# Performance work log

Hardware: AMD Instinct MI355X
Metric: run time of the kernel (lower is better)

Reference implementation:

```python
import jax, jax.numpy as jnp
import numpy as np

N_NODES, N_EDGES = 5000, 50000
NUM_BASIS, CUTOFF, RADIAL_DIM = 8, 5.0, 64
NODE_EMBED, MAX_Z = 64, 100
NUM_NEIGHBORS = 10.0
PI = float(np.pi)

IRREPS_EDGE = [(1, 0, 1), (1, 1, -1), (1, 2, 1)]      # 1x0e + 1x1o + 1x2e (dim 9)
IRREPS_INIT = [(64, 0, 1)]                            # 64x0e
IRREPS_HID  = [(32, 0, 1), (16, 1, -1), (8, 2, 1)]    # 32x0e + 16x1o + 8x2e (dim 120)

def _offsets(irr):
    offs, o = [], 0
    for m, l, p in irr:
        offs.append(o); o += m * (2 * l + 1)
    return offs

def _sh_blocks(v, xp):
    # real spherical harmonics, component normalization, m = -l..l, v must be unit
    x, y, z = v[..., 0], v[..., 1], v[..., 2]
    s3, s5, s15 = 3.0 ** 0.5, 5.0 ** 0.5, 15.0 ** 0.5
    Y0 = xp.ones(v.shape[:-1] + (1,), dtype=v.dtype)
    Y1 = xp.stack([y, z, x], axis=-1) * s3
    Y2 = xp.stack([s15 * x * y, s15 * y * z, 0.5 * s5 * (3.0 * z * z - 1.0),
                   s15 * x * z, 0.5 * s15 * (x * x - y * y)], axis=-1)
    return [Y0, Y1, Y2]

def _rand_rot(rng):
    q, _ = np.linalg.qr(rng.normal(size=(3, 3)))
    if np.linalg.det(q) < 0:
        q[:, 0] = -q[:, 0]
    return q

def _wigner_D(l, R, pts):
    A = _sh_blocks(pts, np)[l]
    B = _sh_blocks(pts @ R.T, np)[l]
    return np.linalg.lstsq(A, B, rcond=None)[0].T  # Y(R r) = D @ Y(r)

def _cg(l1, l2, l3):
    # unit-norm real Clebsch-Gordan tensor from null space of rotation invariance
    rng = np.random.default_rng(1000 + 100 * l1 + 10 * l2 + l3)
    pts = rng.normal(size=(256, 3)); pts /= np.linalg.norm(pts, axis=1, keepdims=True)
    d1, d2, d3 = 2 * l1 + 1, 2 * l2 + 1, 2 * l3 + 1
    rows = []
    for _ in range(3):
        R = _rand_rot(rng)
        K = np.kron(np.kron(_wigner_D(l1, R, pts), _wigner_D(l2, R, pts)), _wigner_D(l3, R, pts))
        rows.append(K - np.eye(d1 * d2 * d3))
    _, _, Vt = np.linalg.svd(np.vstack(rows))
    C = Vt[-1].reshape(d1, d2, d3)
    i = np.argmax(np.abs(C))
    if C.flat[i] < 0:
        C = -C
    return (C / np.linalg.norm(C)).astype(np.float32)

def _make_paths(irreps_in, irreps_out):
    paths, off = [], 0
    fan = [0] * len(irreps_out)
    for i1, (m1, l1, p1) in enumerate(irreps_in):
        for i2, (m2, l2, p2) in enumerate(IRREPS_EDGE):
            for i3, (m3, l3, p3) in enumerate(irreps_out):
                if abs(l1 - l2) <= l3 <= l1 + l2 and p1 * p2 == p3:
                    paths.append((i1, i2, i3, off))
                    off += m1 * m2 * m3
                    fan[i3] += m1 * m2
    return paths, off, fan

PATHS0, NUMEL0, FAN0 = _make_paths(IRREPS_INIT, IRREPS_HID)   # NUMEL0 = 3584
PATHS1, NUMEL1, FAN1 = _make_paths(IRREPS_HID, IRREPS_HID)    # NUMEL1 = 3456

CG = {}
for _paths, _irr_in in ((PATHS0, IRREPS_INIT), (PATHS1, IRREPS_HID)):
    for _i1, _i2, _i3, _ in _paths:
        _key = (_irr_in[_i1][1], IRREPS_EDGE[_i2][1], IRREPS_HID[_i3][1])
        if _key not in CG:
            CG[_key] = jnp.asarray(_cg(*_key))

EDGE_OFF = _offsets(IRREPS_EDGE)

def _tensor_product(x, sh, w, irreps_in, irreps_out, paths, fan):
    E = x.shape[0]
    in_off = _offsets(irreps_in)
    outs = [jnp.zeros((E, m * (2 * l + 1)), x.dtype) for m, l, p in irreps_out]
    for i1, i2, i3, off in paths:
        m1, l1, _ = irreps_in[i1]
        _, l2, _ = IRREPS_EDGE[i2]
        m3, l3, _ = irreps_out[i3]
        x1 = x[:, in_off[i1]:in_off[i1] + m1 * (2 * l1 + 1)].reshape(E, m1, 2 * l1 + 1)
        y = sh[:, EDGE_OFF[i2]:EDGE_OFF[i2] + 2 * l2 + 1]
        wb = w[:, off:off + m1 * m3].reshape(E, m1, m3)
        alpha = (2 * l3 + 1) ** 0.5 / float(fan[i3]) ** 0.5
        msg = jnp.einsum('eui,ej,ijk,euv->evk', x1, y, CG[(l1, l2, l3)], wb) * alpha
        outs[i3] = outs[i3] + msg.reshape(E, -1)
    return jnp.concatenate(outs, axis=1)

def _self_connection(x, ws, irreps_in, irreps_out):
    N = x.shape[0]
    in_off = _offsets(irreps_in)
    outs, wi = [], 0
    for m3, l3, p3 in irreps_out:
        hit = [j for j, (m1, l1, p1) in enumerate(irreps_in) if (l1, p1) == (l3, p3)]
        if hit:
            j = hit[0]
            m1, l1, _ = irreps_in[j]
            xb = x[:, in_off[j]:in_off[j] + m1 * (2 * l1 + 1)].reshape(N, m1, 2 * l1 + 1)
            yb = jnp.einsum('nui,uv->nvi', xb, ws[wi]) / float(m1) ** 0.5
            outs.append(yb.reshape(N, -1)); wi += 1
        else:
            outs.append(jnp.zeros((N, m3 * (2 * l3 + 1)), x.dtype))
    return jnp.concatenate(outs, axis=1)

def _forward(positions, embed, rad_w1, rad_b1, rad_w2, rad_b2,
             wnn0_w1, wnn0_w2, wnn1_w1, wnn1_w2,
             sc0_0e, sc1_0e, sc1_1o, sc1_2e,
             edge_vec, edge_len, atomic_numbers, edge_index):
    node = embed[atomic_numbers]                                  # (N, 64)
    src, dst = edge_index[0], edge_index[1]
    u = edge_vec / (edge_len[:, None] + 1e-8)                     # unit edge vectors
    sh = jnp.concatenate(_sh_blocks(u, jnp), axis=-1)             # (E, 9)
    # radial basis encoding: Bessel basis * smooth cosine cutoff -> MLP
    freqs = jnp.arange(1, NUM_BASIS + 1, dtype=edge_len.dtype) * (PI / CUTOFF)
    r = edge_len[:, None]
    basis = jnp.sin(freqs * r) / jnp.maximum(r, 1e-8)
    xr = edge_len / CUTOFF
    cut = jnp.where(xr < 1.0, 0.5 * (1.0 + jnp.cos(PI * xr)), 0.0)
    rad = jax.nn.silu((basis * cut[:, None]) @ rad_w1 + rad_b1) @ rad_w2 + rad_b2
    inv_sqrt_n = 1.0 / NUM_NEIGHBORS ** 0.5
    layers = [(IRREPS_INIT, PATHS0, FAN0, wnn0_w1, wnn0_w2, [sc0_0e], True),
              (IRREPS_HID, PATHS1, FAN1, wnn1_w1, wnn1_w2, [sc1_0e, sc1_1o, sc1_2e], False)]
    for irr_in, paths, fan, w1, w2, scs, do_act in layers:
        w = jax.nn.silu(rad @ w1) @ w2                            # per-edge TP weights
        msg = _tensor_product(node[src], sh, w, irr_in, IRREPS_HID, paths, fan)
        agg = jax.ops.segment_sum(msg, dst, num_segments=N_NODES) * inv_sqrt_n
        node = agg + _self_connection(node, scs, irr_in, IRREPS_HID)
        if do_act:                                                # silu on L=0 scalars only
            node = jnp.concatenate([jax.nn.silu(node[:, :32]), node[:, 32:]], axis=1)
    return node                                                   # (N, 120)

def setup_inputs():
    key = jax.random.key(0)
    ks = jax.random.split(key, 20)
    edge_vec = jax.random.normal(ks[0], (N_EDGES, 3), jnp.float32) * 1.5
    edge_len = jnp.linalg.norm(edge_vec, axis=-1)
    return {
        'positions': jax.random.normal(ks[1], (N_NODES, 3), jnp.float32) * 5.0,
        'embed': jax.random.normal(ks[2], (MAX_Z, NODE_EMBED), jnp.float32),
        'rad_w1': jax.random.normal(ks[3], (NUM_BASIS, 64), jnp.float32) / NUM_BASIS ** 0.5,
        'rad_b1': jnp.zeros((64,), jnp.float32),
        'rad_w2': jax.random.normal(ks[4], (64, RADIAL_DIM), jnp.float32) / 8.0,
        'rad_b2': jnp.zeros((RADIAL_DIM,), jnp.float32),
        'wnn0_w1': jax.random.normal(ks[5], (RADIAL_DIM, 64), jnp.float32) / 8.0,
        'wnn0_w2': jax.random.normal(ks[6], (64, NUMEL0), jnp.float32) / 8.0,
        'wnn1_w1': jax.random.normal(ks[7], (RADIAL_DIM, 64), jnp.float32) / 8.0,
        'wnn1_w2': jax.random.normal(ks[8], (64, NUMEL1), jnp.float32) / 8.0,
        'sc0_0e': jax.random.normal(ks[9], (64, 32), jnp.float32),
        'sc1_0e': jax.random.normal(ks[10], (32, 32), jnp.float32),
        'sc1_1o': jax.random.normal(ks[11], (16, 16), jnp.float32),
        'sc1_2e': jax.random.normal(ks[12], (8, 8), jnp.float32),
        'edge_vec': edge_vec,
        'edge_len': edge_len,
        'atomic_numbers': jax.random.randint(ks[13], (N_NODES,), 0, MAX_Z, jnp.int32),
        'edge_index': jax.random.randint(ks[14], (2, N_EDGES), 0, N_NODES, jnp.int32),
    }

def reference(positions, embed, rad_w1, rad_b1, rad_w2, rad_b2,
              wnn0_w1, wnn0_w2, wnn1_w1, wnn1_w2,
              sc0_0e, sc1_0e, sc1_1o, sc1_2e,
              edge_vec, edge_len, atomic_numbers, edge_index):
    return _forward(positions, embed, rad_w1, rad_b1, rad_w2, rad_b2,
                    wnn0_w1, wnn0_w2, wnn1_w1, wnn1_w2,
                    sc0_0e, sc1_0e, sc1_1o, sc1_2e,
                    edge_vec, edge_len, atomic_numbers, edge_index)
```

## Files before the change

kernel.cpp:

```cpp
#include <hip/hip_runtime.h>
#include <hip/hip_bf16.h>
#include <math.h>

#define E_EDGES 50000
#define NN 5000

typedef __hip_bfloat16 bf16;
typedef __attribute__((ext_vector_type(8))) short short8;
typedef __attribute__((ext_vector_type(4))) float f32x4;

__device__ __forceinline__ float b2f(bf16 v) { return __bfloat162float(v); }
__device__ __forceinline__ float siluf(float x) { return x / (1.0f + __expf(-x)); }
__device__ __forceinline__ float us2f(unsigned short u) {
  union { unsigned int i; float f; } c; c.i = ((unsigned int)u) << 16; return c.f;
}

__global__ void __launch_bounds__(256) k_setup(
    const float* __restrict__ evec, const float* __restrict__ elen,
    float* __restrict__ shb, float* __restrict__ bc,
    const float* __restrict__ w2, const float* __restrict__ b2,
    const float* __restrict__ w01, const float* __restrict__ w11,
    bf16* __restrict__ Mbb,
    float* __restrict__ bias0, float* __restrict__ bias1,
    const float* __restrict__ emb, const int* __restrict__ an,
    float* __restrict__ node0, bf16* __restrict__ node0b,
    const float* __restrict__ w0, bf16* __restrict__ W0rtb,
    const float* __restrict__ w1w2, bf16* __restrict__ W2t,
    const int* __restrict__ ei, int* __restrict__ hist, int* __restrict__ hist2) {
  const int b = blockIdx.x, tid = threadIdx.x;
  if (b < 196) {
    int e = b*256 + tid;
    if (e >= E_EDGES) return;
    atomicAdd(&hist[ei[e]], 1);
    atomicAdd(&hist2[ei[E_EDGES + e]], 1);
    float x = evec[3*e+0], y = evec[3*e+1], z = evec[3*e+2];
    float r = elen[e];
    float inv = 1.0f / (r + 1e-8f);
    float ux = x*inv, uy = y*inv, uz = z*inv;
    const float s3 = 1.7320508075688772f, s5 = 2.2360679774997896f, s15 = 3.8729833462074170f;
    float* sh = shb + (size_t)e*12;
    sh[0] = 1.0f;
    sh[1] = s3*uy; sh[2] = s3*uz; sh[3] = s3*ux;
    sh[4] = s15*ux*uy; sh[5] = s15*uy*uz; sh[6] = 0.5f*s5*(3.0f*uz*uz - 1.0f);
    sh[7] = s15*ux*uz; sh[8] = 0.5f*s15*(ux*ux - uy*uy);
    sh[9] = 0.f; sh[10] = 0.f; sh[11] = 0.f;
    float rr = fmaxf(r, 1e-8f);
    const float pi = 3.14159265358979f;
    float xr = r * 0.2f;
    float cut = (xr < 1.0f) ? 0.5f*(1.0f + cosf(pi*xr)) : 0.0f;
    float fb = pi * 0.2f;
    for (int k = 1; k <= 8; ++k)
      bc[(size_t)e*8 + (k-1)] = sinf(fb*(float)k*r)/rr * cut;
  } else if (b < 212) {
    int i = (b-196)*256 + tid;
    int hh = i >> 6, c = i & 63;
    float a0 = 0.f, a1 = 0.f;
    for (int j = 0; j < 64; ++j) {
      float wv = w2[hh*64 + j];
      a0 += wv * w01[j*64 + c];
      a1 += wv * w11[j*64 + c];
    }
    Mbb[(size_t)c*64 + hh]        = __float2bfloat16(a0);
    Mbb[(size_t)(64 + c)*64 + hh] = __float2bfloat16(a1);
    if (hh == 0) {
      float s0 = 0.f, s1 = 0.f;
      for (int j = 0; j < 64; ++j) {
        s0 += b2[j] * w01[j*64 + c];
        s1 += b2[j] * w11[j*64 + c];
      }
      bias0[c] = s0;
      bias1[c] = s1;
    }
  } else if (b < 1462) {
    int i = (b-212)*256 + tid;
    int n = i >> 6, c = i & 63;
    float v = emb[an[n]*64 + c];
    node0[i] = v;
    node0b[i] = __float2bfloat16(v);
  } else if (b < 2358) {
    int idx = (b-1462)*256 + tid;
    int col = idx >> 6, u = idx & 63;
    int hh = col / 56, vp = col - hh*56;
    int boff, m3, v;
    if (vp < 32)      { boff = 0;    m3 = 32; v = vp; }
    else if (vp < 48) { boff = 2048; m3 = 16; v = vp - 32; }
    else              { boff = 3072; m3 = 8;  v = vp - 48; }
    W0rtb[idx] = __float2bfloat16(w0[hh*3584 + boff + u*m3 + v]);
  } else {
    int idx = (b-2358)*256 + tid;
    int nn = idx >> 6, k = idx & 63;
    int p, loc;
    if (nn < 1024)      { p=0;  loc=nn;      }
    else if (nn < 1536) { p=1;  loc=nn-1024; }
    else if (nn < 1792) { p=2;  loc=nn-1536; }
    else if (nn < 2048) { p=3;  loc=nn-1792; }
    else if (nn < 2560) { p=4;  loc=nn-2048; }
    else if (nn < 2688) { p=5;  loc=nn-2560; }
    else if (nn < 2944) { p=6;  loc=nn-2688; }
    else if (nn < 3008) { p=7;  loc=nn-2944; }
    else if (nn < 3136) { p=8;  loc=nn-3008; }
    else if (nn < 3392) { p=9;  loc=nn-3136; }
    else                { p=10; loc=nn-3392; }
    const int M1s[11] = {32,32,32,16,16,16,16,8,8,8,8};
    const int M3s[11] = {32,16,8,16,32,8,16,8,16,32,8};
    int m1 = M1s[p], m3 = M3s[p];
    int v = loc / m1, u = loc - v*m1;
    int src = (nn - loc) + u*m3 + v;
    W2t[idx] = __float2bfloat16(w1w2[(size_t)k*3456 + src]);
  }
}

__global__ void __launch_bounds__(256) k_mid(
    const float* __restrict__ bc,
    const float* __restrict__ w1, const float* __restrict__ b1,
    const bf16* __restrict__ Mbb,
    const float* __restrict__ bias0, const float* __restrict__ bias1,
    float* __restrict__ q0, bf16* __restrict__ q1b,
    const int* __restrict__ hist, int* __restrict__ start,
    const int* __restrict__ hist2, int* __restrict__ start2) {
  __shared__ float smem[1024];
  __shared__ __align__(16) short sHb[2048];
  const int tid = threadIdx.x;
  const int b = blockIdx.x;
  if (b < 1563) {
    float* sW1 = smem;
    float* sB  = smem + 512;
    float* sb0 = smem + 576;
    float* sb1 = smem + 640;
    float* sBC = smem + 704;
    const int j = tid >> 6, m = tid & 63;
    for (int i = tid; i < 512; i += 256) sW1[i] = w1[i];
    if (tid < 64) { sB[tid] = b1[tid]; sb0[tid] = bias0[tid]; sb1[tid] = bias1[tid]; }
    {
      int e = b*32 + (tid >> 3);
      int k = tid & 7;
      int eL = e < E_EDGES ? e : E_EDGES-1;
      sBC[tid] = bc[(size_t)eL*8 + k];
    }
    __syncthreads();
    #pragma unroll
    for (int g = 0; g < 8; ++g) {
      int el = g*4 + j;
      float t = sB[m];
      #pragma unroll
      for (int k = 0; k < 8; ++k) t += sBC[el*8+k]*sW1[k*64+m];
      bf16 hv = __float2bfloat16(siluf(t));
      sHb[el*64 + m] = *(short*)&hv;
    }
    __syncthreads();
    const int w = tid >> 6, lane = tid & 63;
    const int row16 = lane & 15, quad = lane >> 4;
    const int mtile = w & 1, cg = w >> 1;
    const short* ap = sHb + (mtile*16 + row16)*64 + quad*8;
    short8 a0 = *(const short8*)ap;
    short8 a1 = *(const short8*)(ap + 32);
    f32x4 acc[4] = {};
    #pragma unroll
    for (int ni = 0; ni < 4; ++ni) {
      const short* bp = (const short*)Mbb + (size_t)(cg*64 + ni*16 + row16)*64 + quad*8;
      short8 b0 = *(const short8*)bp;
      short8 b1v = *(const short8*)(bp + 32);
      acc[ni] = __builtin_amdgcn_mfma_f32_16x16x32_bf16(a0, b0, acc[ni], 0,0,0);
      acc[ni] = __builtin_amdgcn_mfma_f32_16x16x32_bf16(a1, b1v, acc[ni], 0,0,0);
    }
    const float* bias = cg ? sb1 : sb0;
    #pragma unroll
    for (int ni = 0; ni < 4; ++ni) {
      int c = ni*16 + row16;
      float bv = bias[c];
      #pragma unroll
      for (int r = 0; r < 4; ++r) {
        int e = b*32 + mtile*16 + quad*4 + r;
        if (e < E_EDGES) {
          float val = siluf(acc[ni][r] + bv);
          if (cg == 0) q0[(size_t)e*64 + c] = val;
          else         q1b[(size_t)e*64 + c] = __float2bfloat16(val);
        }
      }
    }
  } else {
    const int* h = (b == 1563) ? hist : hist2;
    int* st      = (b == 1563) ? start : start2;
    int* sp = (int*)smem;
    int base = tid*20;
    int localsum = 0;
    for (int i = 0; i < 20; ++i) { int jj = base+i; localsum += (jj < NN) ? h[jj] : 0; }
    sp[tid] = localsum;
    __syncthreads();
    if (tid == 0) {
      int acc = 0;
      for (int i = 0; i < 256; ++i) { int t = sp[i]; sp[i] = acc; acc += t; }
    }
    __syncthreads();
    int run = sp[tid];
    for (int i = 0; i < 20; ++i) {
      int jj = base+i;
      if (jj < NN) { st[jj] = run; run += h[jj]; }
    }
    if (tid == 255) st[NN] = run;
  }
}

__global__ void __launch_bounds__(256) k_pre0(
    const int* __restrict__ ei,
    const int* __restrict__ start, int* __restrict__ cursor, int* __restrict__ perm,
    const int* __restrict__ start2, int* __restrict__ cursor2, int* __restrict__ perm2,
    const bf16* __restrict__ A, const bf16* __restrict__ B, bf16* __restrict__ out) {
  __shared__ short lds[4][32*64];
  const int b = blockIdx.x, tid = threadIdx.x;
  if (b < 196) {
    int e = b*256 + tid;
    if (e >= E_EDGES) return;
    int src = ei[e];
    perm[start[src] + atomicAdd(&cursor[src], 1)] = e;
    int dst = ei[E_EDGES + e];
    perm2[start2[dst] + atomicAdd(&cursor2[dst], 1)] = e;
  } else {
    const int bb = b - 196;
    const int wid = tid >> 6, lane = tid & 63;
    const int nt = (bb % 14)*4 + wid;
    const int r0 = (bb / 14)*32;
    const int row16 = lane & 15, quad = lane >> 4;
    short8 a[2][2];
    #pragma unroll
    for (int mi = 0; mi < 2; ++mi) {
      int r = r0 + mi*16 + row16;
      int rg = (r < NN) ? r : 0;
      const short* ap = (const short*)A + (size_t)rg*64 + quad*8;
      a[mi][0] = *(const short8*)(ap);
      a[mi][1] = *(const short8*)(ap + 32);
    }
    if (nt < 56) {
      f32x4 acc[4][2] = {};
      #pragma unroll
      for (int ni = 0; ni < 4; ++ni) {
        int col = nt*64 + ni*16 + row16;
        const short* bp = (const short*)B + (size_t)col*64 + quad*8;
        short8 b0 = *(const short8*)(bp);
        short8 b1 = *(const short8*)(bp + 32);
        #pragma unroll
        for (int mi = 0; mi < 2; ++mi) {
          acc[ni][mi] = __builtin_amdgcn_mfma_f32_16x16x32_bf16(a[mi][0], b0, acc[ni][mi], 0,0,0);
          acc[ni][mi] = __builtin_amdgcn_mfma_f32_16x16x32_bf16(a[mi][1], b1, acc[ni][mi], 0,0,0);
        }
      }
      #pragma unroll
      for (int ni = 0; ni < 4; ++ni)
        #pragma unroll
        for (int mi = 0; mi < 2; ++mi)
          #pragma unroll
          for (int rr = 0; rr < 4; ++rr) {
            bf16 hv = __float2bfloat16(acc[ni][mi][rr]);
            lds[wid][(mi*16 + quad*4 + rr)*64 + ni*16 + row16] = *(short*)&hv;
          }
    }
    __syncthreads();
    if (nt < 56) {
      #pragma unroll
      for (int it = 0; it < 4; ++it) {
        int unit = it*64 + lane;
        int rrow = unit >> 3;
        int cu = (unit & 7) * 8;
        int r = r0 + rrow;
        if (r < NN)
          *(uint4*)((short*)out + (size_t)r*3584 + nt*64 + cu) =
              *(const uint4*)&lds[wid][rrow*64 + cu];
      }
    }
  }
}

__global__ void __launch_bounds__(256) k_msg0z(
    const float* __restrict__ q0, const bf16* __restrict__ G0,
    const int* __restrict__ start, const int* __restrict__ perm,
    float* __restrict__ zbuf) {
  __shared__ uint4 g4[448];
  __shared__ float sq[4][64];
  const int n = blockIdx.x;
  const int tid = threadIdx.x;
  const int wv = tid >> 6, lane = tid & 63;
  const uint4* gr = (const uint4*)(G0 + (size_t)n*3584);
  for (int i = tid; i < 448; i += 256) g4[i] = gr[i];
  const int s0 = start[n], s1 = start[n+1];
  __syncthreads();
  const short* gs = (const short*)g4;
  for (int base = s0; base < s1; base += 4) {
    int idx = base + wv;
    if (idx < s1) {
      int e = perm[idx];
      sq[wv][lane] = q0[(size_t)e*64 + lane];
      float z = 0.f;
      if (lane < 56) {
        #pragma unroll
        for (int h = 0; h < 64; ++h)
          z += sq[wv][h]*us2f((unsigned short)gs[h*56 + lane]);
        zbuf[(size_t)e*56 + lane] = z;
      }
    }
  }
}

__global__ void k_agg0(const float* __restrict__ zbuf, const float* __restrict__ shb,
                       const int* __restrict__ start2, const int* __restrict__ perm2,
                       const float* __restrict__ node0, const float* __restrict__ sc00,
                       float* __restrict__ node1) {
  __shared__ float n0[64];
  int n = blockIdx.x, tid = threadIdx.x;
  if (tid < 64) n0[tid] = node0[(size_t)n*64 + tid];
  __syncthreads();
  if (tid >= 120) return;
  int c = tid, zi, shi;
  if (c < 32)      { zi = c; shi = -1; }
  else if (c < 80) { int j = c-32, v = j/3, k = j - v*3; zi = 32 + v; shi = 1 + k; }
  else             { int j = c-80, v = j/5, k = j - v*5; zi = 48 + v; shi = 4 + k; }
  float acc = 0.f;
  const int s0 = start2[n], s1 = start2[n+1];
  for (int idx = s0; idx < s1; ++idx) {
    int e = perm2[idx];
    float z = zbuf[(size_t)e*56 + zi];
    acc += (shi < 0) ? z : z*shb[(size_t)e*12 + shi];
  }
  acc *= 0.125f * 0.3162277660168379f;
  if (c < 32) {
    float s = 0.f;
    for (int u = 0; u < 64; ++u) s += n0[u]*sc00[u*32 + c];
    acc += s * 0.125f;
    acc = siluf(acc);
  }
  node1[(size_t)n*120 + c] = acc;
}


static __device__ const int TM1[54] = {
  32,32,32,32,32,32,32,32,32,32,32,32,32,32,32,32,
  32,32,32,32,32,32,32,32,
  32,32,32,32,
  16,16,16,16,
  16,16,16,16,16,16,16,16,
  16,16,
  16,16,16,16,
  8,
  8,8,
  8,8,8,8,
  8};
static __device__ const int TNK[54] = {
  1,1,1,1,1,1,1,1,1,1,1,1,1,1,1,1,
  3,3,3,3,3,3,3,3,
  5,5,5,5,
  3,3,3,3,
  1,1,1,1,1,1,1,1,
  5,5,
  3,3,3,3,
  5,
  3,3,
  1,1,1,1,
  5};
static __device__ const int TTOF[54] = {
  0,0,0,0,0,0,0,0,0,0,0,0,0,0,0,0,
  32,32,32,32,32,32,32,32,
  128,128,128,128,
  288,288,288,288,
  336,336,336,336,336,336,336,336,
  352,352,
  432,432,432,432,
  480,
  520,520,
  544,544,544,544,
  552};
static __device__ const int TOUT[54] = {
  0,2,4,6,8,10,12,14,16,18,20,22,24,26,28,30,
  32,38,44,50,56,62,68,74,
  80,90,100,110,
  32,44,56,68,
  0,4,8,12,16,20,24,28,
  80,100,
  32,44,56,68,
  80,
  32,56,
  0,8,16,24,
  80};

#define US2F(s) us2f((unsigned short)(s))

#define DOT8(wa, wc, t8) \
  (wa[0]*US2F(t8[0]) + wa[1]*US2F(t8[1]) + wa[2]*US2F(t8[2]) + wa[3]*US2F(t8[3]) \
 + wc[0]*US2F(t8[4]) + wc[1]*US2F(t8[5]) + wc[2]*US2F(t8[6]) + wc[3]*US2F(t8[7]))

#define CH32(NKC, HALF) { \
    const int e = lane & 15, uq = lane >> 4; \
    const float* wb = wl + e*32; \
    const int sz = (e & 7) << 2; \
    const short* tb = tls16 + e*600 + toff + uq*8; \
    f32x4 wa = *(const f32x4*)&wb[(uq*8) ^ sz]; \
    f32x4 wc = *(const f32x4*)&wb[(uq*8 + 4) ^ sz]; \
    _Pragma("unroll") \
    for (int k = 0; k < NKC; ++k) { \
      short8 t8 = *(const short8*)(tb + k*32); \
      float ak = DOT8(wa, wc, t8); \
      ak += __shfl_xor(ak, 16); \
      ak += __shfl_xor(ak, 32); \
      if (uq == 0) atomicAdd(&msgl[e*121 + tout + (HALF)*(NKC) + k], ak); \
    } }

#define CH16(NKC, HALF) { \
    const int e = lane & 15, g = lane >> 4; \
    const int vll = g & 1, uh = (g >> 1) << 3; \
    const float* wb = wl + e*32; \
    const int sz = (e & 7) << 2; \
    const short* tb = tls16 + e*600 + toff + uh; \
    f32x4 wa = *(const f32x4*)&wb[(vll*16 + uh) ^ sz]; \
    f32x4 wc = *(const f32x4*)&wb[(vll*16 + uh + 4) ^ sz]; \
    _Pragma("unroll") \
    for (int k = 0; k < NKC; ++k) { \
      short8 t8 = *(const short8*)(tb + k*16); \
      float ak = DOT8(wa, wc, t8); \
      ak += __shfl_xor(ak, 32); \
      if (g < 2) atomicAdd(&msgl[e*121 + tout + ((HALF)*2 + vll)*(NKC) + k], ak); \
    } }

#define CH8(NKC, HALF) { \
    const int e = lane & 15, vll = lane >> 4; \
    const float* wb = wl + e*32; \
    const int sz = (e & 7) << 2; \
    const short* tb = tls16 + e*600 + toff; \
    f32x4 wa = *(const f32x4*)&wb[(vll*8) ^ sz]; \
    f32x4 wc = *(const f32x4*)&wb[(vll*8 + 4) ^ sz]; \
    _Pragma("unroll") \
    for (int k = 0; k < NKC; ++k) { \
      short8 t8 = *(const short8*)(tb + k*8); \
      float ak = DOT8(wa, wc, t8); \
      atomicAdd(&msgl[e*121 + tout + ((HALF)*4 + vll)*(NKC) + k], ak); \
    } }

#define STB(ST, VAL) { bf16 hv_ = __float2bfloat16(VAL); tp[ST] = *(short*)&hv_; }

__global__ void __launch_bounds__(256, 4) k_fuse(
    const bf16* __restrict__ q1b, const bf16* __restrict__ W2t,
    const float* __restrict__ node1, const float* __restrict__ shb,
    const int* __restrict__ ei, float* __restrict__ msg1) {
  __shared__ __align__(16) short tls16[16*600];
  __shared__ __align__(16) float wls[4*512];
  __shared__ float msgl[16*121];
  __shared__ float shl[16*12];
  float* xl = wls;

  const int tid = threadIdx.x;
  const int wv = tid >> 6, lane = tid & 63;
  const int e0 = blockIdx.x * 16;
  const int row16 = lane & 15, quad = lane >> 4;

  {
    int e = tid >> 4, c0 = tid & 15;
    int src = ei[e0 + e];
    const float* xp = node1 + (size_t)src*120;
    for (int c = c0; c < 120; c += 16) xl[e*120 + c] = xp[c];
    if (c0 < 12) shl[e*12 + c0] = shb[(size_t)(e0+e)*12 + c0];
  }
  for (int i = tid; i < 1936; i += 256) msgl[i] = 0.f;

  const short* ap = (const short*)q1b + (size_t)(e0 + row16)*64 + quad*8;
  short8 a0 = *(const short8*)ap;
  short8 a1 = *(const short8*)(ap + 32);

  __syncthreads();

  {
    const float Av = 0.3162277660168379f, Bc = 0.1825741858350554f, B2 = 0.3651483716701107f;
    const int I_[11] = {0,2,0,1,1,2, 0,1,2, 0,2};
    const int J_[11] = {2,0,1,0,2,1, 0,1,2, 0,2};
    const int K_[11] = {0,0,1,1,3,3, 2,2,2, 4,4};
    const float V_[11] = {Av,Av,Av,Av,Av,Av, -Bc,B2,-Bc, -Av,Av};
    const float P = 0.2390457218668787f, Q = 0.2070196678027063f, R = 0.1195228609334394f;
    const int I2_[25] = {0,0,2, 0,0,1,1,3,3, 1,1,2, 1,1,4, 2, 2,3,3, 2,4,4, 3,3,4};
    const int J2_[25] = {0,2,0, 1,3,0,3,0,1, 1,2,1, 1,4,1, 2, 3,2,3, 4,2,4, 3,4,3};
    const int K2_[25] = {2,0,0, 3,1,3,0,1,0, 2,1,1, 4,1,1, 2, 3,3,2, 4,4,2, 4,3,3};
    const float V2_[25] = {P,P,P, -Q,-Q,-Q,-Q,-Q,-Q, -R,-R,-R, Q,Q,Q, -P,
                           -R,-R,-R, P,P,P, -Q,-Q,-Q};

    if (wv == 0) {
      #pragma unroll
      for (int p = 0; p < 12; ++p) {
        int j = p*64 + lane;
        int e = j/48, r = j - e*48;
        int u = r/3, k = r - u*3;
        const float* x = xl + e*120;
        short* tp = tls16 + e*600;
        STB(288 + k*16 + u, x[32+u*3+k]*0.1178511301977579f);
      }
      #pragma unroll
      for (int p = 0; p < 4; ++p) {
        int j = p*64 + lane;
        int e = j >> 4, u = j & 15;
        const float* x = xl + e*120; const float* sh = shl + e*12;
        short* tp = tls16 + e*600;
        STB(336 + u, (x[32+u*3]*sh[1] + x[32+u*3+1]*sh[2] + x[32+u*3+2]*sh[3])
                     * 0.0771516749810460f);
      }
      #pragma unroll
      for (int p = 0; p < 2; ++p) {
        int j = p*64 + lane;
        int e = j >> 3, u = j & 7;
        const float* x = xl + e*120; const float* sh = shl + e*12;
        short* tp = tls16 + e*600;
        float y0 = x[80+u*5], y1 = x[80+u*5+1], y2 = x[80+u*5+2],
              y3 = x[80+u*5+3], y4 = x[80+u*5+4];
        float o0=0.f,o1=0.f,o2=0.f,o3=0.f,o4=0.f;
        #pragma unroll
        for (int q = 0; q < 25; ++q) {
          float xv = (I2_[q]==0) ? y0 : ((I2_[q]==1) ? y1 : ((I2_[q]==2) ? y2 :
                     ((I2_[q]==3) ? y3 : y4)));
          float term = V2_[q]*xv*sh[4+J2_[q]];
          if (K2_[q]==0) o0 += term; else if (K2_[q]==1) o1 += term;
          else if (K2_[q]==2) o2 += term; else if (K2_[q]==3) o3 += term; else o4 += term;
        }
        const float sc = 0.2795084971874737f;
        STB(552 + u, o0*sc); STB(552 + 8 + u, o1*sc); STB(552 + 16 + u, o2*sc);
        STB(552 + 24 + u, o3*sc); STB(552 + 32 + u, o4*sc);
      }
    } else if (wv == 1) {
      #pragma unroll
      for (int p = 0; p < 10; ++p) {
        int j = p*64 + lane;
        int e = j/40, r = j - e*40;
        int u = r/5, k = r - u*5;
        const float* x = xl + e*120;
        short* tp = tls16 + e*600;
        STB(480 + k*8 + u, x[80+u*5+k]*0.125f);
      }
      #pragma unroll
      for (int p = 0; p < 4; ++p) {
        int j = p*64 + lane;
        int e = j >> 4, u = j & 15;
        const float* x = xl + e*120; const float* sh = shl + e*12;
        short* tp = tls16 + e*600;
        float x0 = x[32+u*3], x1 = x[32+u*3+1], x2 = x[32+u*3+2];
        float o0=0.f,o1=0.f,o2=0.f,o3=0.f,o4=0.f;
        #pragma unroll
        for (int q = 0; q < 11; ++q) {
          float xv = (I_[q]==0) ? x0 : ((I_[q]==1) ? x1 : x2);
          float term = V_[q]*xv*sh[1+J_[q]];
          if (K_[q]==0) o0 += term; else if (K_[q]==1) o1 += term;
          else if (K_[q]==2) o2 += term; else if (K_[q]==3) o3 += term; else o4 += term;
        }
        const float sc = 0.2795084971874737f;
        STB(352 + u, o0*sc); STB(352 + 16 + u, o1*sc); STB(352 + 32 + u, o2*sc);
        STB(352 + 48 + u, o3*sc); STB(352 + 64 + u, o4*sc);
      }
      #pragma unroll
      for (int p = 0; p < 2; ++p) {
        int j = p*64 + lane;
        int e = j >> 3, u = j & 7;
        const float* x = xl + e*120; const float* sh = shl + e*12;
        short* tp = tls16 + e*600;
        STB(544 + u, (x[80+u*5]*sh[4] + x[80+u*5+1]*sh[5] + x[80+u*5+2]*sh[6]
                    + x[80+u*5+3]*sh[7] + x[80+u*5+4]*sh[8]) * 0.0597614304667197f);
      }
    } else if (wv == 2) {
      #pragma unroll
      for (int p = 0; p < 8; ++p) {
        int j = p*64 + lane;
        int e = j >> 5, u = j & 31;
        const float* x = xl + e*120;
        short* tp = tls16 + e*600;
        STB(u, x[u] * 0.1336306209562122f);
      }
      #pragma unroll
      for (int p = 0; p < 4; ++p) {
        int j = p*64 + lane;
        int e = j >> 4, u = j & 15;
        const float* x = xl + e*120; const float* sh = shl + e*12;
        short* tp = tls16 + e*600;
        float x0 = x[32+u*3], x1 = x[32+u*3+1], x2 = x[32+u*3+2];
        float o0=0.f,o1=0.f,o2=0.f;
        #pragma unroll
        for (int q = 0; q < 11; ++q) {
          float xv = (I_[q]==0) ? x0 : ((I_[q]==1) ? x1 : x2);
          float term = V_[q]*xv*sh[4+K_[q]];
          if (J_[q]==0) o0 += term; else if (J_[q]==1) o1 += term; else o2 += term;
        }
        const float sc = 0.2041241452319315f;
        STB(432 + u, o0*sc); STB(432 + 16 + u, o1*sc); STB(432 + 32 + u, o2*sc);
      }
      #pragma unroll
      for (int p = 0; p < 2; ++p) {
        int j = p*64 + lane;
        int e = j >> 3, u = j & 7;
        const float* x = xl + e*120; const float* sh = shl + e*12;
        short* tp = tls16 + e*600;
        float y0 = x[80+u*5], y1 = x[80+u*5+1], y2 = x[80+u*5+2],
              y3 = x[80+u*5+3], y4 = x[80+u*5+4];
        float o0=0.f,o1=0.f,o2=0.f;
        #pragma unroll
        for (int q = 0; q < 11; ++q) {
          float xv = (K_[q]==0) ? y0 : ((K_[q]==1) ? y1 : ((K_[q]==2) ? y2 :
                     ((K_[q]==3) ? y3 : y4)));
          float term = V_[q]*xv*sh[1+I_[q]];
          if (J_[q]==0) o0 += term; else if (J_[q]==1) o1 += term; else o2 += term;
        }
        const float sc = 0.2041241452319315f;
        STB(520 + u, o0*sc); STB(520 + 8 + u, o1*sc); STB(520 + 16 + u, o2*sc);
      }
    } else {
      #pragma unroll
      for (int p = 0; p < 8; ++p) {
        int j = p*64 + lane;
        int e = j >> 5, u = j & 31;
        const float* x = xl + e*120; const float* sh = shl + e*12;
        short* tp = tls16 + e*600;
        float xu = x[u];
        #pragma unroll
        for (int k = 0; k < 3; ++k)
          STB(32 + k*32 + u, xu*sh[1+k]*0.1178511301977579f);
      }
      #pragma unroll
      for (int p = 0; p < 8; ++p) {
        int j = p*64 + lane;
        int e = j >> 5, u = j & 31;
        const float* x = xl + e*120; const float* sh = shl + e*12;
        short* tp = tls16 + e*600;
        float xu = x[u];
        #pragma unroll
        for (int k = 0; k < 5; ++k)
          STB(128 + k*32 + u, xu*sh[4+k]*0.125f);
      }
    }
  }
  __syncthreads();

  float* wl = wls + wv*512;

  short8 bf0[4], bf1[4];
  {
    const int ntp = wv;
    #pragma unroll
    for (int ni = 0; ni < 4; ++ni) {
      const short* bp = (const short*)W2t + (size_t)(ntp*64 + ni*16 + row16)*64 + quad*8;
      bf0[ni] = *(const short8*)bp;
      bf1[ni] = *(const short8*)(bp + 32);
    }
  }

  for (int nt = wv; nt < 54; nt += 4) {
    f32x4 acc[4] = {};
    #pragma unroll
    for (int ni = 0; ni < 4; ++ni) {
      acc[ni] = __builtin_amdgcn_mfma_f32_16x16x32_bf16(a0, bf0[ni], acc[ni], 0,0,0);
      acc[ni] = __builtin_amdgcn_mfma_f32_16x16x32_bf16(a1, bf1[ni], acc[ni], 0,0,0);
    }
    if (nt + 4 < 54) {
      #pragma unroll
      for (int ni = 0; ni < 4; ++ni) {
        const short* bp = (const short*)W2t + (size_t)((nt+4)*64 + ni*16 + row16)*64 + quad*8;
        bf0[ni] = *(const short8*)bp;
        bf1[ni] = *(const short8*)(bp + 32);
      }
    }
    const int m1 = TM1[nt], nk = TNK[nt], toff = TTOF[nt], tout = TOUT[nt];
    #pragma unroll
    for (int half = 0; half < 2; ++half) {
      #pragma unroll
      for (int nh = 0; nh < 2; ++nh) {
        const int ni = half*2 + nh;
        #pragma unroll
        for (int r = 0; r < 4; ++r) {
          int e = quad*4 + r;
          int ch = nh*16 + row16;
          wl[e*32 + (ch ^ ((e & 7) << 2))] = acc[ni][r];
        }
      }
      if (m1 == 32) {
        if (nk == 1)      CH32(1, half)
        else if (nk == 3) CH32(3, half)
        else              CH32(5, half)
      } else if (m1 == 16) {
        if (nk == 1)      CH16(1, half)
        else if (nk == 3) CH16(3, half)
        else              CH16(5, half)
      } else {
        if (nk == 1)      CH8(1, half)
        else if (nk == 3) CH8(3, half)
        else              CH8(5, half)
      }
    }
  }

  __syncthreads();
  const float s = 0.3162277660168379f;
  for (int i = tid; i < 1920; i += 256) {
    int e = i / 120, c = i - e*120;
    msg1[(size_t)e0*120 + i] = msgl[e*121 + c] * s;
  }
}

__global__ void k_out(const float* __restrict__ msg1,
                      const int* __restrict__ start2, const int* __restrict__ perm2,
                      const float* __restrict__ node1,
                      const float* __restrict__ sc0e, const float* __restrict__ sc1o,
                      const float* __restrict__ sc2e, float* __restrict__ out) {
  __shared__ float x[120];
  int n = blockIdx.x, tid = threadIdx.x;
  if (tid < 120) x[tid] = node1[(size_t)n*120 + tid];
  __syncthreads();
  if (tid >= 120) return;
  float v = 0.f;
  const int s0 = start2[n], s1 = start2[n+1];
  for (int idx = s0; idx < s1; ++idx)
    v += msg1[(size_t)perm2[idx]*120 + tid];
  if (tid < 32) {
    float s = 0.f;
    for (int u = 0; u < 32; ++u) s += x[u]*sc0e[u*32 + tid];
    v += s * 0.1767766952966369f;
  } else if (tid < 80) {
    int jj = tid - 32, vv = jj/3, k = jj - vv*3;
    float s = 0.f;
    for (int u = 0; u < 16; ++u) s += x[32 + u*3 + k]*sc1o[u*16 + vv];
    v += s * 0.25f;
  } else {
    int jj = tid - 80, vv = jj/5, k = jj - vv*5;
    float s = 0.f;
    for (int u = 0; u < 8; ++u) s += x[80 + u*5 + k]*sc2e[u*8 + vv];
    v += s * 0.3535533905932738f;
  }
  out[(size_t)n*120 + tid] = v;
}

extern "C" void kernel_launch(void* const* d_in, const int* in_sizes, int n_in,
                              void* d_out, int out_size, void* d_ws, size_t ws_size,
                              hipStream_t stream) {
  const float* embed   = (const float*)d_in[1];
  const float* rad_w1  = (const float*)d_in[2];
  const float* rad_b1  = (const float*)d_in[3];
  const float* rad_w2  = (const float*)d_in[4];
  const float* rad_b2  = (const float*)d_in[5];
  const float* wnn0_w1 = (const float*)d_in[6];
  const float* wnn0_w2 = (const float*)d_in[7];
  const float* wnn1_w1 = (const float*)d_in[8];
  const float* wnn1_w2 = (const float*)d_in[9];
  const float* sc0_0e  = (const float*)d_in[10];
  const float* sc1_0e  = (const float*)d_in[11];
  const float* sc1_1o  = (const float*)d_in[12];
  const float* sc1_2e  = (const float*)d_in[13];
  const float* edge_vec = (const float*)d_in[14];
  const float* edge_len = (const float*)d_in[15];
  const int*  anum    = (const int*)d_in[16];
  const int*  ei      = (const int*)d_in[17];

  float* ws = (float*)d_ws;
  float* shbuf = ws;
  float* bc    = ws + 600000;
  bf16*  q1b   = (bf16*)(ws + 1000000);
  float* node0 = ws + 2600000;
  bf16*  node0b= (bf16*)(ws + 2920000);
  bf16*  W0rtb = (bf16*)(ws + 3080000);
  bf16*  W2t   = (bf16*)(ws + 3194688);
  bf16*  Mbb   = (bf16*)(ws + 3305280);
  float* bias0 = ws + 3309376;
  float* bias1 = ws + 3309440;
  int*   hist   = (int*)(ws + 3309504);
  int*   cursor = (int*)(ws + 3314504);
  int*   hist2  = (int*)(ws + 3319504);
  int*   cursor2= (int*)(ws + 3324504);
  int*   start  = (int*)(ws + 3329504);
  int*   start2 = (int*)(ws + 3334512);
  int*   perm   = (int*)(ws + 3339520);
  int*   perm2  = (int*)(ws + 3389520);
  float* node1 = ws + 3439520;
  float* msg1  = ws + 4039520;
  float* q0    = ws + 10039520;
  float* zbuf  = ws + 13239520;
  bf16*  G0    = (bf16*)(ws + 16039520);

  hipMemsetAsync(hist, 0, 20000*sizeof(int), stream);

  k_setup<<<3222, 256, 0, stream>>>(edge_vec, edge_len, shbuf, bc,
                                    rad_w2, rad_b2, wnn0_w1, wnn1_w1, Mbb, bias0, bias1,
                                    embed, anum, node0, node0b,
                                    wnn0_w2, W0rtb, wnn1_w2, W2t, ei, hist, hist2);
  k_mid<<<1565, 256, 0, stream>>>(bc, rad_w1, rad_b1, Mbb, bias0, bias1,
                                  q0, q1b, hist, start, hist2, start2);
  k_pre0<<<196 + 14*157, 256, 0, stream>>>(ei, start, cursor, perm,
                                           start2, cursor2, perm2,
                                           node0b, W0rtb, G0);
  k_msg0z<<<NN, 256, 0, stream>>>(q0, G0, start, perm, zbuf);
  k_agg0<<<NN, 128, 0, stream>>>(zbuf, shbuf, start2, perm2, node0, sc0_0e, node1);

  k_fuse<<<3125, 256, 0, stream>>>(q1b, W2t, node1, shbuf, ei, msg1);

  k_out<<<NN, 128, 0, stream>>>(msg1, start2, perm2, node1, sc1_0e, sc1_1o, sc1_2e, (float*)d_out);
}
```

Baseline: 408.5 us.

## Use fp16 dot2 contractions and software-pipeline MFMA tiles in k_fuse

Result: slower. 577.6 us (+41.4%).

```diff
diff --git a/kernel.cpp b/kernel.cpp
--- a/kernel.cpp
+++ b/kernel.cpp
@@ -8,11 +8,27 @@
 typedef __hip_bfloat16 bf16;
 typedef __attribute__((ext_vector_type(8))) short short8;
 typedef __attribute__((ext_vector_type(4))) float f32x4;
+typedef __attribute__((ext_vector_type(2))) _Float16 h2;
 
 __device__ __forceinline__ float b2f(bf16 v) { return __bfloat162float(v); }
 __device__ __forceinline__ float siluf(float x) { return x / (1.0f + __expf(-x)); }
 __device__ __forceinline__ float us2f(unsigned short u) {
   union { unsigned int i; float f; } c; c.i = ((unsigned int)u) << 16; return c.f;
+}
+
+__device__ __forceinline__ float fdot2f(h2 a, h2 b, float c) {
+#if __has_builtin(__builtin_amdgcn_fdot2)
+  return __builtin_amdgcn_fdot2(a, b, c, false);
+#else
+  return c + (float)a.x*(float)b.x + (float)a.y*(float)b.y;
+#endif
+}
+__device__ __forceinline__ float dot8h(uint4 w, uint4 t, float acc) {
+  acc = fdot2f(__builtin_bit_cast(h2, w.x), __builtin_bit_cast(h2, t.x), acc);
+  acc = fdot2f(__builtin_bit_cast(h2, w.y), __builtin_bit_cast(h2, t.y), acc);
+  acc = fdot2f(__builtin_bit_cast(h2, w.z), __builtin_bit_cast(h2, t.z), acc);
+  acc = fdot2f(__builtin_bit_cast(h2, w.w), __builtin_bit_cast(h2, t.w), acc);
+  return acc;
 }
 
 __global__ void __launch_bounds__(256) k_setup(
@@ -380,69 +396,81 @@
   0,8,16,24,
   80};
 
-#define US2F(s) us2f((unsigned short)(s))
-
-#define DOT8(wa, wc, t8) \
-  (wa[0]*US2F(t8[0]) + wa[1]*US2F(t8[1]) + wa[2]*US2F(t8[2]) + wa[3]*US2F(t8[3]) \
- + wc[0]*US2F(t8[4]) + wc[1]*US2F(t8[5]) + wc[2]*US2F(t8[6]) + wc[3]*US2F(t8[7]))
-
-#define CH32(NKC, HALF) { \
-    const int e = lane & 15, uq = lane >> 4; \
-    const float* wb = wl + e*32; \
-    const int sz = (e & 7) << 2; \
-    const short* tb = tls16 + e*600 + toff + uq*8; \
-    f32x4 wa = *(const f32x4*)&wb[(uq*8) ^ sz]; \
-    f32x4 wc = *(const f32x4*)&wb[(uq*8 + 4) ^ sz]; \
+#define STB(ST, VAL) { _Float16 hv_ = (_Float16)(VAL); tp[ST] = *(short*)&hv_; }
+
+#define STORE_WL(ACC) { \
     _Pragma("unroll") \
-    for (int k = 0; k < NKC; ++k) { \
-      short8 t8 = *(const short8*)(tb + k*32); \
-      float ak = DOT8(wa, wc, t8); \
-      ak += __shfl_xor(ak, 16); \
+    for (int ni_ = 0; ni_ < 4; ++ni_) { \
+      _Pragma("unroll") \
+      for (int r_ = 0; r_ < 4; ++r_) { \
+        int e_ = quad*4 + r_; \
+        int c_ = ni_*16 + row16; \
+        _Float16 hv_ = (_Float16)((ACC)[ni_][r_]); \
+        wl16[e_*64 + ((((c_>>3) ^ (e_&7))<<3) | (c_&7))] = *(short*)&hv_; \
+      } \
+    } }
+
+#define MFMA_STORE(NTT) { \
+    f32x4 acc_[4] = {}; \
+    _Pragma("unroll") \
+    for (int ni_ = 0; ni_ < 4; ++ni_) { \
+      acc_[ni_] = __builtin_amdgcn_mfma_f32_16x16x32_bf16(a0, bf0[ni_], acc_[ni_], 0,0,0); \
+      acc_[ni_] = __builtin_amdgcn_mfma_f32_16x16x32_bf16(a1, bf1[ni_], acc_[ni_], 0,0,0); \
+    } \
+    if ((NTT) + 4 < 54) { \
+      _Pragma("unroll") \
+      for (int ni_ = 0; ni_ < 4; ++ni_) { \
+        const short* bp_ = (const short*)W2t + (size_t)(((NTT)+4)*64 + ni_*16 + row16)*64 + quad*8; \
+        bf0[ni_] = *(const short8*)bp_; \
+        bf1[ni_] = *(const short8*)(bp_ + 32); \
+      } \
+    } \
+    STORE_WL(acc_) }
+
+#define LD2(NKC, STRIDE) \
+    _Pragma("unroll") \
+    for (int k_ = 0; k_ < NKC; ++k_) { \
+      tr[k_][0] = *(const uint4*)&tb[k_*(STRIDE)]; \
+      tr[k_][1] = *(const uint4*)&tb[k_*(STRIDE) + 8]; \
+    }
+#define LD1(NKC) \
+    _Pragma("unroll") \
+    for (int k_ = 0; k_ < NKC; ++k_) \
+      tr[k_][0] = *(const uint4*)&tb[k_*8];
+
+#define CP32(NKC) \
+    _Pragma("unroll") \
+    for (int k_ = 0; k_ < NKC; ++k_) { \
+      float ak = dot8h(wr0, tr[k_][0], 0.f); \
+      ak = dot8h(wr1, tr[k_][1], ak); \
       ak += __shfl_xor(ak, 32); \
-      if (uq == 0) atomicAdd(&msgl[e*121 + tout + (HALF)*(NKC) + k], ak); \
-    } }
-
-#define CH16(NKC, HALF) { \
-    const int e = lane & 15, g = lane >> 4; \
-    const int vll = g & 1, uh = (g >> 1) << 3; \
-    const float* wb = wl + e*32; \
-    const int sz = (e & 7) << 2; \
-    const short* tb = tls16 + e*600 + toff + uh; \
-    f32x4 wa = *(const f32x4*)&wb[(vll*16 + uh) ^ sz]; \
-    f32x4 wc = *(const f32x4*)&wb[(vll*16 + uh + 4) ^ sz]; \
+      if (g < 2) atomicAdd(&msgl[e*121 + tout + (g&1)*(NKC) + k_], ak); \
+    }
+#define CP16(NKC) \
     _Pragma("unroll") \
-    for (int k = 0; k < NKC; ++k) { \
-      short8 t8 = *(const short8*)(tb + k*16); \
-      float ak = DOT8(wa, wc, t8); \
-      ak += __shfl_xor(ak, 32); \
-      if (g < 2) atomicAdd(&msgl[e*121 + tout + ((HALF)*2 + vll)*(NKC) + k], ak); \
-    } }
-
-#define CH8(NKC, HALF) { \
-    const int e = lane & 15, vll = lane >> 4; \
-    const float* wb = wl + e*32; \
-    const int sz = (e & 7) << 2; \
-    const short* tb = tls16 + e*600 + toff; \
-    f32x4 wa = *(const f32x4*)&wb[(vll*8) ^ sz]; \
-    f32x4 wc = *(const f32x4*)&wb[(vll*8 + 4) ^ sz]; \
+    for (int k_ = 0; k_ < NKC; ++k_) { \
+      float ak = dot8h(wr0, tr[k_][0], 0.f); \
+      ak = dot8h(wr1, tr[k_][1], ak); \
+      atomicAdd(&msgl[e*121 + tout + g*(NKC) + k_], ak); \
+    }
+#define CP8(NKC) \
     _Pragma("unroll") \
-    for (int k = 0; k < NKC; ++k) { \
-      short8 t8 = *(const short8*)(tb + k*8); \
-      float ak = DOT8(wa, wc, t8); \
-      atomicAdd(&msgl[e*121 + tout + ((HALF)*4 + vll)*(NKC) + k], ak); \
-    } }
-
-#define STB(ST, VAL) { bf16 hv_ = __float2bfloat16(VAL); tp[ST] = *(short*)&hv_; }
+    for (int k_ = 0; k_ < NKC; ++k_) { \
+      float ak = dot8h(wr0, tr[k_][0], 0.f); \
+      atomicAdd(&msgl[e*121 + tout + g*(NKC) + k_], ak); \
+      float ak2 = dot8h(wr1, tr[k_][0], 0.f); \
+      atomicAdd(&msgl[e*121 + tout + (g+4)*(NKC) + k_], ak2); \
+    }
 
 __global__ void __launch_bounds__(256, 4) k_fuse(
     const bf16* __restrict__ q1b, const bf16* __restrict__ W2t,
     const float* __restrict__ node1, const float* __restrict__ shb,
     const int* __restrict__ ei, float* __restrict__ msg1) {
   __shared__ __align__(16) short tls16[16*600];
-  __shared__ __align__(16) float wls[4*512];
+  __shared__ __align__(16) short wls16[4*1024];
   __shared__ float msgl[16*121];
   __shared__ float shl[16*12];
-  float* xl = wls;
+  float* xl = (float*)wls16;
 
   const int tid = threadIdx.x;
   const int wv = tid >> 6, lane = tid & 63;
@@ -461,6 +489,13 @@
   const short* ap = (const short*)q1b + (size_t)(e0 + row16)*64 + quad*8;
   short8 a0 = *(const short8*)ap;
   short8 a1 = *(const short8*)(ap + 32);
+  short8 bf0[4], bf1[4];
+  #pragma unroll
+  for (int ni = 0; ni < 4; ++ni) {
+    const short* bp = (const short*)W2t + (size_t)(wv*64 + ni*16 + row16)*64 + quad*8;
+    bf0[ni] = *(const short8*)bp;
+    bf1[ni] = *(const short8*)(bp + 32);
+  }
 
   __syncthreads();
 
@@ -627,60 +662,55 @@
   }
   __syncthreads();
 
-  float* wl = wls + wv*512;
-
-  short8 bf0[4], bf1[4];
-  {
-    const int ntp = wv;
-    #pragma unroll
-    for (int ni = 0; ni < 4; ++ni) {
-      const short* bp = (const short*)W2t + (size_t)(ntp*64 + ni*16 + row16)*64 + quad*8;
-      bf0[ni] = *(const short8*)bp;
-      bf1[ni] = *(const short8*)(bp + 32);
-    }
-  }
+  short* wl16 = wls16 + wv*1024;
+
+  MFMA_STORE(wv)
 
   for (int nt = wv; nt < 54; nt += 4) {
-    f32x4 acc[4] = {};
-    #pragma unroll
-    for (int ni = 0; ni < 4; ++ni) {
-      acc[ni] = __builtin_amdgcn_mfma_f32_16x16x32_bf16(a0, bf0[ni], acc[ni], 0,0,0);
-      acc[ni] = __builtin_amdgcn_mfma_f32_16x16x32_bf16(a1, bf1[ni], acc[ni], 0,0,0);
-    }
-    if (nt + 4 < 54) {
-      #pragma unroll
-      for (int ni = 0; ni < 4; ++ni) {
-        const short* bp = (const short*)W2t + (size_t)((nt+4)*64 + ni*16 + row16)*64 + quad*8;
-        bf0[ni] = *(const short8*)bp;
-        bf1[ni] = *(const short8*)(bp + 32);
-      }
-    }
     const int m1 = TM1[nt], nk = TNK[nt], toff = TTOF[nt], tout = TOUT[nt];
-    #pragma unroll
-    for (int half = 0; half < 2; ++half) {
-      #pragma unroll
-      for (int nh = 0; nh < 2; ++nh) {
-        const int ni = half*2 + nh;
-        #pragma unroll
-        for (int r = 0; r < 4; ++r) {
-          int e = quad*4 + r;
-          int ch = nh*16 + row16;
-          wl[e*32 + (ch ^ ((e & 7) << 2))] = acc[ni][r];
-        }
-      }
-      if (m1 == 32) {
-        if (nk == 1)      CH32(1, half)
-        else if (nk == 3) CH32(3, half)
-        else              CH32(5, half)
-      } else if (m1 == 16) {
-        if (nk == 1)      CH16(1, half)
-        else if (nk == 3) CH16(3, half)
-        else              CH16(5, half)
-      } else {
-        if (nk == 1)      CH8(1, half)
-        else if (nk == 3) CH8(3, half)
-        else              CH8(5, half)
-      }
+    const int e = lane & 15, g = lane >> 4, e7 = e & 7;
+    const short* wb = wl16 + e*64;
+    uint4 wr0, wr1;
+    uint4 tr[5][2];
+
+    if (m1 == 32) {
+      const int b0 = (g & 1)*4 + ((g >> 1) << 1);
+      wr0 = *(const uint4*)&wb[((b0 ^ e7) << 3)];
+      wr1 = *(const uint4*)&wb[(((b0+1) ^ e7) << 3)];
+      const short* tb = tls16 + e*600 + toff + ((g >> 1) << 4);
+      if (nk == 1)      { LD2(1,32) }
+      else if (nk == 3) { LD2(3,32) }
+      else              { LD2(5,32) }
+    } else if (m1 == 16) {
+      wr0 = *(const uint4*)&wb[(((g*2)   ^ e7) << 3)];
+      wr1 = *(const uint4*)&wb[(((g*2+1) ^ e7) << 3)];
+      const short* tb = tls16 + e*600 + toff;
+      if (nk == 1)      { LD2(1,16) }
+      else if (nk == 3) { LD2(3,16) }
+      else              { LD2(5,16) }
+    } else {
+      wr0 = *(const uint4*)&wb[((g ^ e7) << 3)];
+      wr1 = *(const uint4*)&wb[(((g+4) ^ e7) << 3)];
+      const short* tb = tls16 + e*600 + toff;
+      if (nk == 1)      { LD1(1) }
+      else if (nk == 3) { LD1(3) }
+      else              { LD1(5) }
+    }
+
+    if (nt + 4 < 54) { MFMA_STORE(nt + 4) }
+
+    if (m1 == 32) {
+      if (nk == 1)      { CP32(1) }
+      else if (nk == 3) { CP32(3) }
+      else              { CP32(5) }
+    } else if (m1 == 16) {
+      if (nk == 1)      { CP16(1) }
+      else if (nk == 3) { CP16(3) }
+      else              { CP16(5) }
+    } else {
+      if (nk == 1)      { CP8(1) }
+      else if (nk == 3) { CP8(3) }
+      else              { CP8(5) }
     }
   }
 
```
